# Kernel optimization log

Hardware: AMD Instinct MI355X
Metric: run time of the kernel (lower is better)

## Reference

```python
import jax, jax.numpy as jnp
import numpy as np

N = 100000
E = 1600000
IN_CH = 128
HID = 32
HEADS = 4
OUT_CH = 64
NEG_SLOPE = 0.2


def _gat_conv(x, src, dst, W, att_src, att_dst, bias, heads, out_ch):
    # PyG GATConv (concat=True, add_self_loops handled by caller via src/dst)
    n = x.shape[0]
    xp = (x @ W).reshape(n, heads, out_ch)                  # [N,H,C]
    a_src = (xp * att_src).sum(-1)                          # [N,H]
    a_dst = (xp * att_dst).sum(-1)                          # [N,H]
    e = jax.nn.leaky_relu(a_src[src] + a_dst[dst], NEG_SLOPE)  # [E,H]
    m = jax.ops.segment_max(e, dst, num_segments=n)         # per-dst max (safe: self-loops)
    ex = jnp.exp(e - m[dst])
    denom = jax.ops.segment_sum(ex, dst, num_segments=n)
    alpha = ex / denom[dst]                                  # [E,H]
    out = jax.ops.segment_sum(xp[src] * alpha[:, :, None], dst, num_segments=n)
    return out.reshape(n, heads * out_ch) + bias


def setup_inputs() -> dict:
    key = jax.random.key(0)
    ks = jax.random.split(key, 12)
    sc1 = 1.0 / np.sqrt(IN_CH)
    sc2 = 1.0 / np.sqrt(HID * HEADS * 2)
    return {
        "x_ppi": jax.random.normal(ks[0], (N, IN_CH), jnp.float32),
        "x_go": jax.random.normal(ks[1], (N, IN_CH), jnp.float32),
        "edge_index": jax.random.randint(ks[2], (2, E), 0, N, jnp.int32),
        "W1": jax.random.normal(ks[3], (IN_CH, HEADS * HID), jnp.float32) * sc1,
        "att_src1": jax.random.normal(ks[4], (HEADS, HID), jnp.float32) * sc1,
        "att_dst1": jax.random.normal(ks[5], (HEADS, HID), jnp.float32) * sc1,
        "b1": jnp.zeros((HEADS * HID,), jnp.float32),
        "W2": jax.random.normal(ks[6], (HID * HEADS * 2, OUT_CH), jnp.float32) * sc2,
        "att_src2": jax.random.normal(ks[7], (1, OUT_CH), jnp.float32) * sc2,
        "att_dst2": jax.random.normal(ks[8], (1, OUT_CH), jnp.float32) * sc2,
        "b2": jnp.zeros((OUT_CH,), jnp.float32),
    }


def reference(x_ppi, x_go, edge_index, W1, att_src1, att_dst1, b1, W2, att_src2, att_dst2, b2):
    loops = jnp.arange(N, dtype=edge_index.dtype)
    src = jnp.concatenate([edge_index[0], loops])
    dst = jnp.concatenate([edge_index[1], loops])
    h_ppi = _gat_conv(x_ppi, src, dst, W1, att_src1, att_dst1, b1, HEADS, HID)
    h_go = _gat_conv(x_go, src, dst, W1, att_src1, att_dst1, b1, HEADS, HID)
    h = jax.nn.relu(jnp.concatenate([h_ppi, h_go], axis=-1))  # [N, 2*H*HID]
    out = _gat_conv(h, src, dst, W2, att_src2, att_dst2, b2, 1, OUT_CH)
    return out
```

## Files before the change

kernel.cpp:

```cpp
#include <hip/hip_runtime.h>
#include <hip/hip_fp16.h>

constexpr int NN = 100000;
constexpr int EE = 1600000;
constexpr int ET = EE + NN;
constexpr int EQ = EE / 4;
constexpr int TQ = ET / 4;
constexpr int NBUK = (NN + 255) / 256;
constexpr int PB = 416;
constexpr float NEG = 0.2f;

typedef _Float16 f16x8 __attribute__((ext_vector_type(8)));
typedef _Float16 f16x4 __attribute__((ext_vector_type(4)));
typedef float    f32x4 __attribute__((ext_vector_type(4)));

__global__ __launch_bounds__(256) void k_bcount(const int4* __restrict__ dst4v,
                                                int* __restrict__ bucketCount) {
    __shared__ int bh[NBUK];
    for (int i = threadIdx.x; i < NBUK; i += 256) bh[i] = 0;
    __syncthreads();
    int gtid = blockIdx.x * 256 + threadIdx.x;
    for (int q = gtid; q < TQ; q += PB * 256) {
        int4 d;
        if (q < EQ) {
            d = dst4v[q];
        } else {
            int s0 = (q - EQ) * 4;
            d.x = s0; d.y = s0 + 1; d.z = s0 + 2; d.w = s0 + 3;
        }
        atomicAdd(&bh[d.x >> 8], 1);
        atomicAdd(&bh[d.y >> 8], 1);
        atomicAdd(&bh[d.z >> 8], 1);
        atomicAdd(&bh[d.w >> 8], 1);
    }
    __syncthreads();
    for (int i = threadIdx.x; i < NBUK; i += 256)
        if (bh[i]) atomicAdd(&bucketCount[i], bh[i]);
}

__global__ __launch_bounds__(512) void k_bscan(const int* __restrict__ bucketCount,
                                               int* __restrict__ bstart, int* __restrict__ gcur,
                                               int* __restrict__ rs) {
    __shared__ int sh[512];
    int t = threadIdx.x;
    int v = (t < NBUK) ? bucketCount[t] : 0;
    sh[t] = v;
    __syncthreads();
    for (int o = 1; o < 512; o <<= 1) {
        int u = (t >= o) ? sh[t - o] : 0;
        __syncthreads();
        sh[t] += u;
        __syncthreads();
    }
    if (t < NBUK) { bstart[t] = sh[t] - v; gcur[t] = sh[t] - v; }
    if (t == 0) { bstart[NBUK] = ET; rs[NN] = ET; }
}

__global__ __launch_bounds__(256) void k_bplace(const int4* __restrict__ src4v, const int4* __restrict__ dst4v,
                                                int* __restrict__ gcur, unsigned int* __restrict__ ebuf) {
    __shared__ int bh[NBUK];
    __shared__ int bbase[NBUK];
    for (int i = threadIdx.x; i < NBUK; i += 256) bh[i] = 0;
    __syncthreads();
    int gtid = blockIdx.x * 256 + threadIdx.x;

    int esrc[16];
    int emeta[16];
#pragma unroll
    for (int it = 0; it < 4; it++) {
        int q = gtid + it * (PB * 256);
        bool valid = q < TQ;
        int4 s, d;
        if (valid) {
            if (q < EQ) { s = src4v[q]; d = dst4v[q]; }
            else { int s0 = (q - EQ) * 4; s.x = s0; s.y = s0 + 1; s.z = s0 + 2; s.w = s0 + 3; d = s; }
        } else {
            s.x = s.y = s.z = s.w = 0; d = s;
        }
        int ss[4] = {s.x, s.y, s.z, s.w};
        int dd[4] = {d.x, d.y, d.z, d.w};
#pragma unroll
        for (int k = 0; k < 4; k++) {
            int idx = it * 4 + k;
            if (valid) {
                int b = dd[k] >> 8, l = dd[k] & 255;
                int r = atomicAdd(&bh[b], 1);
                esrc[idx]  = ss[k];
                emeta[idx] = (b << 21) | (l << 13) | r;
            } else {
                emeta[idx] = -1;
            }
        }
    }
    __syncthreads();
    for (int i = threadIdx.x; i < NBUK; i += 256)
        bbase[i] = bh[i] ? atomicAdd(&gcur[i], bh[i]) : 0;
    __syncthreads();
#pragma unroll
    for (int e = 0; e < 16; e++) {
        int me = emeta[e];
        if (me >= 0) {
            int b = me >> 21, l = (me >> 13) & 255, r = me & 8191;
            ebuf[bbase[b] + r] = ((unsigned)l << 24) | (unsigned)esrc[e];
        }
    }
}

__global__ __launch_bounds__(256) void k_csr(const unsigned int* __restrict__ ebuf,
                                             const int* __restrict__ bstart,
                                             int* __restrict__ rs, int* __restrict__ csr) {
    __shared__ int hist[256];
    __shared__ int sh[256];
    __shared__ int cur[256];
    int b = blockIdx.x;
    int t = threadIdx.x;
    int e0 = bstart[b], e1 = bstart[b + 1];
    hist[t] = 0;
    __syncthreads();
    for (int j = e0 + t; j < e1; j += 256)
        atomicAdd(&hist[ebuf[j] >> 24], 1);
    __syncthreads();
    int v = hist[t];
    sh[t] = v;
    __syncthreads();
    for (int o = 1; o < 256; o <<= 1) {
        int u = (t >= o) ? sh[t - o] : 0;
        __syncthreads();
        sh[t] += u;
        __syncthreads();
    }
    int excl = sh[t] - v;
    cur[t] = excl;
    int v0 = b * 256;
    if (v0 + t < NN) rs[v0 + t] = e0 + excl;
    __syncthreads();
    for (int j = e0 + t; j < e1; j += 256) {
        unsigned int e = ebuf[j];
        int l = (int)(e >> 24);
        int r = atomicAdd(&cur[l], 1);
        csr[e0 + r] = (int)(e & 0x00FFFFFFu);
    }
}

template <int K, int C, int OUT_MODE, bool SRCF32>
__global__ __launch_bounds__(256) void gemm_mfma(const void* __restrict__ xv, const float* __restrict__ W,
                                                 __half* __restrict__ xp, int n, int set_off) {
    constexpr int KC  = 64;
    constexpr int AST = KC + 8;
    constexpr int NT  = C / 16;
    constexpr int NST = K / KC;
    __shared__ _Float16 a_lds[128 * AST];
    __shared__ _Float16 w_lds[C * AST];

    const int tid  = threadIdx.x;
    const int w    = tid >> 6;
    const int lane = tid & 63;
    const int quad = lane >> 4;
    const int l16  = lane & 15;
    const long r0  = (long)blockIdx.x * 128;

    f32x4 acc[2][NT];
#pragma unroll
    for (int s = 0; s < 2; s++)
#pragma unroll
        for (int t = 0; t < NT; t++) acc[s][t] = (f32x4){0.f, 0.f, 0.f, 0.f};

    for (int st = 0; st < NST; ++st) {
        const int k0 = st * KC;
        for (int i = tid; i < 128 * (KC / 4); i += 256) {
            int r = i / (KC / 4);
            int q = i % (KC / 4);
            long row = r0 + r;
            f16x4 hv = (f16x4){0, 0, 0, 0};
            if (row < n) {
                if (SRCF32) {
                    float4 v = ((const float4*)xv)[row * (K / 4) + (k0 / 4) + q];
                    hv = (f16x4){(_Float16)v.x, (_Float16)v.y, (_Float16)v.z, (_Float16)v.w};
                } else {
                    hv = ((const f16x4*)xv)[row * (K / 4) + (k0 / 4) + q];
                }
            }
            *(f16x4*)&a_lds[r * AST + q * 4] = hv;
        }
        for (int i = tid; i < C * (KC / 4); i += 256) {
            int nn = i / (KC / 4);
            int kq = i % (KC / 4);
            f16x4 hv;
            hv.x = (_Float16)W[(long)(k0 + kq * 4 + 0) * C + nn];
            hv.y = (_Float16)W[(long)(k0 + kq * 4 + 1) * C + nn];
            hv.z = (_Float16)W[(long)(k0 + kq * 4 + 2) * C + nn];
            hv.w = (_Float16)W[(long)(k0 + kq * 4 + 3) * C + nn];
            *(f16x4*)&w_lds[nn * AST + kq * 4] = hv;
        }
        __syncthreads();

#pragma unroll
        for (int ks = 0; ks < KC; ks += 32) {
            f16x8 a0 = *(const f16x8*)&a_lds[(w * 32 + l16) * AST + ks + quad * 8];
            f16x8 a1 = *(const f16x8*)&a_lds[(w * 32 + 16 + l16) * AST + ks + quad * 8];
#pragma unroll
            for (int t = 0; t < NT; t++) {
                f16x8 b = *(const f16x8*)&w_lds[(t * 16 + l16) * AST + ks + quad * 8];
                acc[0][t] = __builtin_amdgcn_mfma_f32_16x16x32_f16(a0, b, acc[0][t], 0, 0, 0);
                acc[1][t] = __builtin_amdgcn_mfma_f32_16x16x32_f16(a1, b, acc[1][t], 0, 0, 0);
            }
        }
        __syncthreads();
    }

#pragma unroll
    for (int sub = 0; sub < 2; sub++) {
        long rb = r0 + w * 32 + sub * 16 + quad * 4;
#pragma unroll
        for (int t = 0; t < NT; t++) {
            int c = t * 16 + l16;
#pragma unroll
            for (int rg = 0; rg < 4; rg++) {
                long row = rb + rg;
                if (row < n) {
                    __half hv = __float2half(acc[sub][t][rg]);
                    if (OUT_MODE == 0)
                        xp[row * 256 + ((c >> 1) << 2) + (c & 1) + set_off] = hv;
                    else
                        xp[row * (long)C + c] = hv;
                }
            }
        }
    }
}

__global__ __launch_bounds__(256) void attn1_plain(const __half2* __restrict__ xp_p,
                                                   const __half2* __restrict__ xp_g,
                                                   const float* __restrict__ as_w, const float* __restrict__ ad_w,
                                                   float* __restrict__ att_sp, float* __restrict__ att_dp,
                                                   float* __restrict__ att_sg, float* __restrict__ att_dg, int n) {
    int idx = blockIdx.x * 256 + threadIdx.x;
    if (idx >= n * 4) return;
    int v = idx >> 2, hh = idx & 3;
    const __half2* rp = xp_p + (long)v * 64 + hh * 16;
    const __half2* rg = xp_g + (long)v * 64 + hh * 16;
    const float* a1 = as_w + hh * 32;
    const float* a2 = ad_w + hh * 32;
    float sp1 = 0.f, sp2 = 0.f, sg1 = 0.f, sg2 = 0.f;
#pragma unroll
    for (int t = 0; t < 16; t++) {
        float2 fp = __half22float2(rp[t]);
        float2 fg = __half22float2(rg[t]);
        float2 w1 = *(const float2*)(a1 + 2 * t);
        float2 w2 = *(const float2*)(a2 + 2 * t);
        sp1 += fp.x * w1.x + fp.y * w1.y;
        sp2 += fp.x * w2.x + fp.y * w2.y;
        sg1 += fg.x * w1.x + fg.y * w1.y;
        sg2 += fg.x * w2.x + fg.y * w2.y;
    }
    att_sp[idx] = sp1; att_dp[idx] = sp2;
    att_sg[idx] = sg1; att_dg[idx] = sg2;
}

__global__ __launch_bounds__(256) void attn2_kernel(const __half2* __restrict__ xp,
                                                    const float* __restrict__ as_w, const float* __restrict__ ad_w,
                                                    float* __restrict__ asrc, float* __restrict__ adst, int n) {
    int v = blockIdx.x * 256 + threadIdx.x;
    if (v >= n) return;
    const __half2* p = xp + (long)v * 32;
    float s1 = 0.f, s2 = 0.f;
#pragma unroll
    for (int c = 0; c < 32; c++) {
        float2 xv = __half22float2(p[c]);
        float2 w1 = *(const float2*)(as_w + 2 * c);
        float2 w2 = *(const float2*)(ad_w + 2 * c);
        s1 += xv.x * w1.x + xv.y * w1.y;
        s2 += xv.x * w2.x + xv.y * w2.y;
    }
    asrc[v] = s1;
    adst[v] = s2;
}

__global__ __launch_bounds__(256) void w1prep_node(const int* __restrict__ rs, const int* __restrict__ csr,
                                                   const float4* __restrict__ att_sp4, const float4* __restrict__ att_dp4,
                                                   const float4* __restrict__ att_sg4, const float4* __restrict__ att_dg4,
                                                   float4* __restrict__ wbp4, float4* __restrict__ wbg4) {
    int v = blockIdx.x * 16 + (threadIdx.x >> 4);
    if (v >= NN) return;
    int sl = threadIdx.x & 15;
    int e0 = rs[v], e1 = rs[v + 1];
    float4 dp = att_dp4[v], dg = att_dg4[v];
    auto w = [](float e) { e = (e > 0.f) ? e : NEG * e; return __expf(e); };
    for (int j = e0 + sl; j < e1; j += 16) {
        int s = csr[j];
        float4 sp = att_sp4[s], sg = att_sg4[s];
        float4 wp, wg;
        wp.x = w(sp.x + dp.x); wp.y = w(sp.y + dp.y);
        wp.z = w(sp.z + dp.z); wp.w = w(sp.w + dp.w);
        wg.x = w(sg.x + dg.x); wg.y = w(sg.y + dg.y);
        wg.z = w(sg.z + dg.z); wg.w = w(sg.w + dg.w);
        wbp4[j] = wp;
        wbg4[j] = wg;
    }
}

__global__ __launch_bounds__(256) void conv1_pass(const int* __restrict__ rs, const int* __restrict__ csr,
                                                  const uint4* __restrict__ xp,
                                                  const float* __restrict__ wb,
                                                  const float* __restrict__ bias,
                                                  __half* __restrict__ out, int off) {
    int v = blockIdx.x * 4 + (threadIdx.x >> 6);
    if (v >= NN) return;
    int lane = threadIdx.x & 63;
    int qw = lane >> 4;
    int m = lane & 15;
    int hd = m >> 2;
    int e0 = rs[v], e1 = rs[v + 1];

    float a[8];
#pragma unroll
    for (int i = 0; i < 8; i++) a[i] = 0.f;
    float d = 0.f;

    int j = e0;
    for (; j + 16 <= e1; j += 16) {
        int s[4]; float w[4]; uint4 r[4];
#pragma unroll
        for (int k = 0; k < 4; k++) s[k] = csr[j + 4 * k + qw];
#pragma unroll
        for (int k = 0; k < 4; k++) w[k] = wb[(j + 4 * k + qw) * 4 + hd];
#pragma unroll
        for (int k = 0; k < 4; k++) r[k] = xp[(long)s[k] * 16 + m];
#pragma unroll
        for (int k = 0; k < 4; k++) {
            d += w[k];
            float2 f0 = __half22float2(*(__half2*)&r[k].x);
            float2 f1 = __half22float2(*(__half2*)&r[k].y);
            float2 f2 = __half22float2(*(__half2*)&r[k].z);
            float2 f3 = __half22float2(*(__half2*)&r[k].w);
            a[0] += w[k] * f0.x; a[1] += w[k] * f0.y;
            a[2] += w[k] * f1.x; a[3] += w[k] * f1.y;
            a[4] += w[k] * f2.x; a[5] += w[k] * f2.y;
            a[6] += w[k] * f3.x; a[7] += w[k] * f3.y;
        }
    }
    for (; j < e1; j += 4) {
        int jj = j + qw;
        int jc = (jj < e1) ? jj : (e1 - 1);
        int s = csr[jc];
        float w = (jj < e1) ? wb[jc * 4 + hd] : 0.f;
        uint4 r = xp[(long)s * 16 + m];
        d += w;
        float2 f0 = __half22float2(*(__half2*)&r.x);
        float2 f1 = __half22float2(*(__half2*)&r.y);
        float2 f2 = __half22float2(*(__half2*)&r.z);
        float2 f3 = __half22float2(*(__half2*)&r.w);
        a[0] += w * f0.x; a[1] += w * f0.y;
        a[2] += w * f1.x; a[3] += w * f1.y;
        a[4] += w * f2.x; a[5] += w * f2.y;
        a[6] += w * f3.x; a[7] += w * f3.y;
    }

#pragma unroll
    for (int i = 0; i < 8; i++) {
        a[i] += __shfl_xor(a[i], 16);
        a[i] += __shfl_xor(a[i], 32);
    }
    d += __shfl_xor(d, 16);
    d += __shfl_xor(d, 32);

    if (qw == 0) {
        float inv = 1.0f / d;
        const float4* b4 = (const float4*)bias;
        float4 bA = b4[2 * m], bB = b4[2 * m + 1];
        __half2 o01 = __floats2half2_rn(fmaxf(a[0] * inv + bA.x, 0.f), fmaxf(a[1] * inv + bA.y, 0.f));
        __half2 o23 = __floats2half2_rn(fmaxf(a[2] * inv + bA.z, 0.f), fmaxf(a[3] * inv + bA.w, 0.f));
        __half2 o45 = __floats2half2_rn(fmaxf(a[4] * inv + bB.x, 0.f), fmaxf(a[5] * inv + bB.y, 0.f));
        __half2 o67 = __floats2half2_rn(fmaxf(a[6] * inv + bB.z, 0.f), fmaxf(a[7] * inv + bB.w, 0.f));
        uint4 st;
        st.x = *(unsigned int*)&o01;
        st.y = *(unsigned int*)&o23;
        st.z = *(unsigned int*)&o45;
        st.w = *(unsigned int*)&o67;
        *(uint4*)(out + (long)v * 256 + off + 8 * m) = st;
    }
}

__global__ __launch_bounds__(256) void conv2_edge(const int* __restrict__ rs, const int* __restrict__ csr,
                                                  const __half* __restrict__ xp,
                                                  const float* __restrict__ asrc,
                                                  const float* __restrict__ adst,
                                                  const float* __restrict__ bias,
                                                  float* __restrict__ out) {
    int v = blockIdx.x * 4 + (threadIdx.x >> 6);
    if (v >= NN) return;
    int lane = threadIdx.x & 63;
    int qw = lane >> 4;
    int m = lane & 15;
    int e0 = rs[v], e1 = rs[v + 1];
    const uint2* xp2 = (const uint2*)xp;

    float adv = adst[v];
    auto lrexp = [](float e) { e = (e > 0.f) ? e : NEG * e; return __expf(e); };

    float a0 = 0.f, a1 = 0.f, a2 = 0.f, a3 = 0.f, d = 0.f;

    int j = e0;
    for (; j + 16 <= e1; j += 16) {
        int s[4]; float av[4]; uint2 r[4];
#pragma unroll
        for (int k = 0; k < 4; k++) s[k] = csr[j + 4 * k + qw];
#pragma unroll
        for (int k = 0; k < 4; k++) av[k] = asrc[s[k]];
#pragma unroll
        for (int k = 0; k < 4; k++) r[k] = xp2[(long)s[k] * 16 + m];
#pragma unroll
        for (int k = 0; k < 4; k++) {
            float w = lrexp(av[k] + adv);
            d += w;
            float2 x01 = __half22float2(*(__half2*)&r[k].x);
            float2 x23 = __half22float2(*(__half2*)&r[k].y);
            a0 += w * x01.x; a1 += w * x01.y;
            a2 += w * x23.x; a3 += w * x23.y;
        }
    }
    for (; j < e1; j += 4) {
        int jj = j + qw;
        int jc = (jj < e1) ? jj : (e1 - 1);
        int s = csr[jc];
        float av = asrc[s];
        uint2 r = xp2[(long)s * 16 + m];
        float w = (jj < e1) ? lrexp(av + adv) : 0.f;
        d += w;
        float2 x01 = __half22float2(*(__half2*)&r.x);
        float2 x23 = __half22float2(*(__half2*)&r.y);
        a0 += w * x01.x; a1 += w * x01.y;
        a2 += w * x23.x; a3 += w * x23.y;
    }

    a0 += __shfl_xor(a0, 16); a1 += __shfl_xor(a1, 16);
    a2 += __shfl_xor(a2, 16); a3 += __shfl_xor(a3, 16);
    d  += __shfl_xor(d, 16);
    a0 += __shfl_xor(a0, 32); a1 += __shfl_xor(a1, 32);
    a2 += __shfl_xor(a2, 32); a3 += __shfl_xor(a3, 32);
    d  += __shfl_xor(d, 32);

    if (qw == 0) {
        float inv = 1.0f / d;
        float4 b4 = *(const float4*)&bias[4 * m];
        float4 o;
        o.x = a0 * inv + b4.x;
        o.y = a1 * inv + b4.y;
        o.z = a2 * inv + b4.z;
        o.w = a3 * inv + b4.w;
        *(float4*)&out[(long)v * 64 + 4 * m] = o;
    }
}

extern "C" void kernel_launch(void* const* d_in, const int* in_sizes, int n_in,
                              void* d_out, int out_size, void* d_ws, size_t ws_size,
                              hipStream_t stream) {
    const float* x_ppi = (const float*)d_in[0];
    const float* x_go  = (const float*)d_in[1];
    const int*   ei    = (const int*)d_in[2];
    const float* W1    = (const float*)d_in[3];
    const float* as1   = (const float*)d_in[4];
    const float* ad1   = (const float*)d_in[5];
    const float* b1    = (const float*)d_in[6];
    const float* W2    = (const float*)d_in[7];
    const float* as2   = (const float*)d_in[8];
    const float* ad2   = (const float*)d_in[9];
    const float* b2    = (const float*)d_in[10];
    float* out = (float*)d_out;

    char* ws = (char*)d_ws;
    size_t off = 0;
    auto alloc = [&](size_t bytes) -> void* {
        void* p = ws + off;
        off = (off + bytes + 255) & ~(size_t)255;
        return p;
    };
    int* bucketCount = (int*)alloc((size_t)NBUK * 4);
    int* bstart      = (int*)alloc((size_t)(NBUK + 1) * 4);
    int* gcur        = (int*)alloc((size_t)NBUK * 4);
    unsigned int* ebuf = (unsigned int*)alloc((size_t)ET * 4);
    int* rs      = (int*)alloc((size_t)(NN + 1) * 4);
    int* csr     = (int*)alloc((size_t)ET * 4);
    __half* xp_p = (__half*)alloc((size_t)NN * 128 * 2);
    __half* xp_g = (__half*)alloc((size_t)NN * 128 * 2);
    __half* xp2  = (__half*)alloc((size_t)NN * 64 * 2);
    float* attsp = (float*)alloc((size_t)NN * 4 * 4);
    float* attdp = (float*)alloc((size_t)NN * 4 * 4);
    float* attsg = (float*)alloc((size_t)NN * 4 * 4);
    float* attdg = (float*)alloc((size_t)NN * 4 * 4);
    float* asr2  = (float*)alloc((size_t)NN * 4);
    float* ads2  = (float*)alloc((size_t)NN * 4);
    float* wbp   = (float*)alloc((size_t)ET * 16);
    float* wbg   = (float*)alloc((size_t)ET * 16);
    __half* hbuf = (__half*)alloc((size_t)NN * 256 * 2);
    (void)ws_size; (void)in_sizes; (void)n_in; (void)out_size;

    const int GB = (NN + 127) / 128;

    hipMemsetAsync(bucketCount, 0, (size_t)NBUK * 4, stream);
    k_bcount<<<PB, 256, 0, stream>>>((const int4*)(ei + EE), bucketCount);
    k_bscan<<<1, 512, 0, stream>>>(bucketCount, bstart, gcur, rs);
    k_bplace<<<PB, 256, 0, stream>>>((const int4*)ei, (const int4*)(ei + EE), gcur, ebuf);
    k_csr<<<NBUK, 256, 0, stream>>>(ebuf, bstart, rs, csr);

    gemm_mfma<128, 128, 1, true><<<GB, 256, 0, stream>>>(x_ppi, W1, xp_p, NN, 0);
    gemm_mfma<128, 128, 1, true><<<GB, 256, 0, stream>>>(x_go, W1, xp_g, NN, 0);
    attn1_plain<<<(NN * 4 + 255) / 256, 256, 0, stream>>>((const __half2*)xp_p, (const __half2*)xp_g,
                                                          as1, ad1, attsp, attdp, attsg, attdg, NN);
    w1prep_node<<<(NN + 15) / 16, 256, 0, stream>>>(rs, csr, (const float4*)attsp, (const float4*)attdp,
                                                    (const float4*)attsg, (const float4*)attdg,
                                                    (float4*)wbp, (float4*)wbg);
    conv1_pass<<<NN / 4, 256, 0, stream>>>(rs, csr, (const uint4*)xp_p, wbp, b1, hbuf, 0);
    conv1_pass<<<NN / 4, 256, 0, stream>>>(rs, csr, (const uint4*)xp_g, wbg, b1, hbuf, 128);

    gemm_mfma<256, 64, 1, false><<<GB, 256, 0, stream>>>(hbuf, W2, xp2, NN, 0);
    attn2_kernel<<<(NN + 255) / 256, 256, 0, stream>>>((const __half2*)xp2, as2, ad2, asr2, ads2, NN);
    conv2_edge<<<NN / 4, 256, 0, stream>>>(rs, csr, xp2, asr2, ads2, b2, out);
}
```

Before: 563.0 us.

## Fuse attention logits into direct-load MFMA GEMM with pre-transposed fp16 weights

Replaces the LDS-staged GEMM with one that loads A fragments and pre-transposed fp16 weights straight from global memory into MFMA registers. A small prep kernel transposes and converts W1/W2 once per call. The per-node attention dot products are computed in the GEMM epilogue from the fp32 accumulators via lane shuffles, which removes the separate attn1/attn2 kernels and their re-read of xp. The trade-off is that weights are now read per block from global memory or L2 rather than from LDS, and the attention logits use fp32 accumulators instead of fp16-rounded xp.

Measured after the change: 505.7 us. -10.2%, faster.

```diff
diff --git a/kernel.cpp b/kernel.cpp
--- a/kernel.cpp
+++ b/kernel.cpp
@@ -142,22 +142,35 @@
     }
 }
 
-template <int K, int C, int OUT_MODE, bool SRCF32>
-__global__ __launch_bounds__(256) void gemm_mfma(const void* __restrict__ xv, const float* __restrict__ W,
-                                                 __half* __restrict__ xp, int n, int set_off) {
-    constexpr int KC  = 64;
-    constexpr int AST = KC + 8;
-    constexpr int NT  = C / 16;
-    constexpr int NST = K / KC;
-    __shared__ _Float16 a_lds[128 * AST];
-    __shared__ _Float16 w_lds[C * AST];
-
+__global__ __launch_bounds__(256) void k_wprep(const float* __restrict__ W1, const float* __restrict__ W2,
+                                               _Float16* __restrict__ w1T, _Float16* __restrict__ w2T) {
+    int idx = blockIdx.x * 256 + threadIdx.x;
+    if (idx < 128 * 128) {
+        int nn = idx >> 7, k = idx & 127;
+        w1T[idx] = (_Float16)W1[k * 128 + nn];
+    }
+    int i2 = idx - 128 * 128;
+    if (i2 >= 0 && i2 < 64 * 256) {
+        int nn = i2 >> 8, k = i2 & 255;
+        w2T[i2] = (_Float16)W2[k * 64 + nn];
+    }
+}
+
+template <int K, int C, bool SRCF32, int AMODE>
+__global__ __launch_bounds__(256) void gemm_direct(const void* __restrict__ xv,
+                                                   const _Float16* __restrict__ wT,
+                                                   const float* __restrict__ as_w, const float* __restrict__ ad_w,
+                                                   __half* __restrict__ xp,
+                                                   float* __restrict__ att_s, float* __restrict__ att_d, int n) {
+    constexpr int NT = C / 16;
     const int tid  = threadIdx.x;
     const int w    = tid >> 6;
     const int lane = tid & 63;
     const int quad = lane >> 4;
     const int l16  = lane & 15;
     const long r0  = (long)blockIdx.x * 128;
+    const long row0 = r0 + w * 32 + l16;
+    const long row1 = row0 + 16;
 
     f32x4 acc[2][NT];
 #pragma unroll
@@ -165,115 +178,112 @@
 #pragma unroll
         for (int t = 0; t < NT; t++) acc[s][t] = (f32x4){0.f, 0.f, 0.f, 0.f};
 
-    for (int st = 0; st < NST; ++st) {
-        const int k0 = st * KC;
-        for (int i = tid; i < 128 * (KC / 4); i += 256) {
-            int r = i / (KC / 4);
-            int q = i % (KC / 4);
-            long row = r0 + r;
-            f16x4 hv = (f16x4){0, 0, 0, 0};
-            if (row < n) {
-                if (SRCF32) {
-                    float4 v = ((const float4*)xv)[row * (K / 4) + (k0 / 4) + q];
-                    hv = (f16x4){(_Float16)v.x, (_Float16)v.y, (_Float16)v.z, (_Float16)v.w};
-                } else {
-                    hv = ((const f16x4*)xv)[row * (K / 4) + (k0 / 4) + q];
+#pragma unroll
+    for (int ks = 0; ks < K; ks += 32) {
+        f16x8 a0 = (f16x8){0, 0, 0, 0, 0, 0, 0, 0};
+        f16x8 a1 = (f16x8){0, 0, 0, 0, 0, 0, 0, 0};
+        if (SRCF32) {
+            if (row0 < n) {
+                const float4* p = (const float4*)((const float*)xv + row0 * K + ks) + quad * 2;
+                float4 u = p[0], v = p[1];
+                a0 = (f16x8){(_Float16)u.x, (_Float16)u.y, (_Float16)u.z, (_Float16)u.w,
+                             (_Float16)v.x, (_Float16)v.y, (_Float16)v.z, (_Float16)v.w};
+            }
+            if (row1 < n) {
+                const float4* p = (const float4*)((const float*)xv + row1 * K + ks) + quad * 2;
+                float4 u = p[0], v = p[1];
+                a1 = (f16x8){(_Float16)u.x, (_Float16)u.y, (_Float16)u.z, (_Float16)u.w,
+                             (_Float16)v.x, (_Float16)v.y, (_Float16)v.z, (_Float16)v.w};
+            }
+        } else {
+            if (row0 < n) a0 = *(const f16x8*)((const _Float16*)xv + row0 * K + ks + quad * 8);
+            if (row1 < n) a1 = *(const f16x8*)((const _Float16*)xv + row1 * K + ks + quad * 8);
+        }
+#pragma unroll
+        for (int t = 0; t < NT; t++) {
+            f16x8 b = *(const f16x8*)(wT + (long)(t * 16 + l16) * K + ks + quad * 8);
+            acc[0][t] = __builtin_amdgcn_mfma_f32_16x16x32_f16(a0, b, acc[0][t], 0, 0, 0);
+            acc[1][t] = __builtin_amdgcn_mfma_f32_16x16x32_f16(a1, b, acc[1][t], 0, 0, 0);
+        }
+    }
+
+#pragma unroll
+    for (int sub = 0; sub < 2; sub++) {
+        long rb = r0 + w * 32 + sub * 16 + quad * 4;
+#pragma unroll
+        for (int t = 0; t < NT; t++) {
+            int c = t * 16 + l16;
+#pragma unroll
+            for (int rg = 0; rg < 4; rg++) {
+                long row = rb + rg;
+                if (row < n) xp[row * (long)C + c] = __float2half(acc[sub][t][rg]);
+            }
+        }
+    }
+
+    if (AMODE == 1) {
+        float asw[8], adw[8];
+#pragma unroll
+        for (int t = 0; t < 8; t++) {
+            int ci = (t >> 1) * 32 + (t & 1) * 16 + l16;
+            asw[t] = as_w[ci];
+            adw[t] = ad_w[ci];
+        }
+#pragma unroll
+        for (int sub = 0; sub < 2; sub++) {
+#pragma unroll
+            for (int rg = 0; rg < 4; rg++) {
+                long row = r0 + w * 32 + sub * 16 + quad * 4 + rg;
+                float hs[4] = {0.f, 0.f, 0.f, 0.f};
+                float hd[4] = {0.f, 0.f, 0.f, 0.f};
+#pragma unroll
+                for (int t = 0; t < 8; t++) {
+                    float av = acc[sub][t][rg];
+                    hs[t >> 1] += av * asw[t];
+                    hd[t >> 1] += av * adw[t];
+                }
+#pragma unroll
+                for (int h = 0; h < 4; h++) {
+                    hs[h] += __shfl_xor(hs[h], 1); hs[h] += __shfl_xor(hs[h], 2);
+                    hs[h] += __shfl_xor(hs[h], 4); hs[h] += __shfl_xor(hs[h], 8);
+                    hd[h] += __shfl_xor(hd[h], 1); hd[h] += __shfl_xor(hd[h], 2);
+                    hd[h] += __shfl_xor(hd[h], 4); hd[h] += __shfl_xor(hd[h], 8);
+                }
+                if (l16 == 0 && row < n) {
+                    ((float4*)att_s)[row] = make_float4(hs[0], hs[1], hs[2], hs[3]);
+                    ((float4*)att_d)[row] = make_float4(hd[0], hd[1], hd[2], hd[3]);
                 }
             }
-            *(f16x4*)&a_lds[r * AST + q * 4] = hv;
-        }
-        for (int i = tid; i < C * (KC / 4); i += 256) {
-            int nn = i / (KC / 4);
-            int kq = i % (KC / 4);
-            f16x4 hv;
-            hv.x = (_Float16)W[(long)(k0 + kq * 4 + 0) * C + nn];
-            hv.y = (_Float16)W[(long)(k0 + kq * 4 + 1) * C + nn];
-            hv.z = (_Float16)W[(long)(k0 + kq * 4 + 2) * C + nn];
-            hv.w = (_Float16)W[(long)(k0 + kq * 4 + 3) * C + nn];
-            *(f16x4*)&w_lds[nn * AST + kq * 4] = hv;
-        }
-        __syncthreads();
-
-#pragma unroll
-        for (int ks = 0; ks < KC; ks += 32) {
-            f16x8 a0 = *(const f16x8*)&a_lds[(w * 32 + l16) * AST + ks + quad * 8];
-            f16x8 a1 = *(const f16x8*)&a_lds[(w * 32 + 16 + l16) * AST + ks + quad * 8];
-#pragma unroll
-            for (int t = 0; t < NT; t++) {
-                f16x8 b = *(const f16x8*)&w_lds[(t * 16 + l16) * AST + ks + quad * 8];
-                acc[0][t] = __builtin_amdgcn_mfma_f32_16x16x32_f16(a0, b, acc[0][t], 0, 0, 0);
-                acc[1][t] = __builtin_amdgcn_mfma_f32_16x16x32_f16(a1, b, acc[1][t], 0, 0, 0);
-            }
-        }
-        __syncthreads();
-    }
-
-#pragma unroll
-    for (int sub = 0; sub < 2; sub++) {
-        long rb = r0 + w * 32 + sub * 16 + quad * 4;
+        }
+    }
+    if (AMODE == 2) {
+        float asw[NT], adw[NT];
 #pragma unroll
         for (int t = 0; t < NT; t++) {
-            int c = t * 16 + l16;
+            asw[t] = as_w[t * 16 + l16];
+            adw[t] = ad_w[t * 16 + l16];
+        }
+#pragma unroll
+        for (int sub = 0; sub < 2; sub++) {
 #pragma unroll
             for (int rg = 0; rg < 4; rg++) {
-                long row = rb + rg;
-                if (row < n) {
-                    __half hv = __float2half(acc[sub][t][rg]);
-                    if (OUT_MODE == 0)
-                        xp[row * 256 + ((c >> 1) << 2) + (c & 1) + set_off] = hv;
-                    else
-                        xp[row * (long)C + c] = hv;
+                long row = r0 + w * 32 + sub * 16 + quad * 4 + rg;
+                float s = 0.f, d = 0.f;
+#pragma unroll
+                for (int t = 0; t < NT; t++) {
+                    float av = acc[sub][t][rg];
+                    s += av * asw[t];
+                    d += av * adw[t];
+                }
+                s += __shfl_xor(s, 1); s += __shfl_xor(s, 2); s += __shfl_xor(s, 4); s += __shfl_xor(s, 8);
+                d += __shfl_xor(d, 1); d += __shfl_xor(d, 2); d += __shfl_xor(d, 4); d += __shfl_xor(d, 8);
+                if (l16 == 0 && row < n) {
+                    att_s[row] = s;
+                    att_d[row] = d;
                 }
             }
         }
     }
-}
-
-__global__ __launch_bounds__(256) void attn1_plain(const __half2* __restrict__ xp_p,
-                                                   const __half2* __restrict__ xp_g,
-                                                   const float* __restrict__ as_w, const float* __restrict__ ad_w,
-                                                   float* __restrict__ att_sp, float* __restrict__ att_dp,
-                                                   float* __restrict__ att_sg, float* __restrict__ att_dg, int n) {
-    int idx = blockIdx.x * 256 + threadIdx.x;
-    if (idx >= n * 4) return;
-    int v = idx >> 2, hh = idx & 3;
-    const __half2* rp = xp_p + (long)v * 64 + hh * 16;
-    const __half2* rg = xp_g + (long)v * 64 + hh * 16;
-    const float* a1 = as_w + hh * 32;
-    const float* a2 = ad_w + hh * 32;
-    float sp1 = 0.f, sp2 = 0.f, sg1 = 0.f, sg2 = 0.f;
-#pragma unroll
-    for (int t = 0; t < 16; t++) {
-        float2 fp = __half22float2(rp[t]);
-        float2 fg = __half22float2(rg[t]);
-        float2 w1 = *(const float2*)(a1 + 2 * t);
-        float2 w2 = *(const float2*)(a2 + 2 * t);
-        sp1 += fp.x * w1.x + fp.y * w1.y;
-        sp2 += fp.x * w2.x + fp.y * w2.y;
-        sg1 += fg.x * w1.x + fg.y * w1.y;
-        sg2 += fg.x * w2.x + fg.y * w2.y;
-    }
-    att_sp[idx] = sp1; att_dp[idx] = sp2;
-    att_sg[idx] = sg1; att_dg[idx] = sg2;
-}
-
-__global__ __launch_bounds__(256) void attn2_kernel(const __half2* __restrict__ xp,
-                                                    const float* __restrict__ as_w, const float* __restrict__ ad_w,
-                                                    float* __restrict__ asrc, float* __restrict__ adst, int n) {
-    int v = blockIdx.x * 256 + threadIdx.x;
-    if (v >= n) return;
-    const __half2* p = xp + (long)v * 32;
-    float s1 = 0.f, s2 = 0.f;
-#pragma unroll
-    for (int c = 0; c < 32; c++) {
-        float2 xv = __half22float2(p[c]);
-        float2 w1 = *(const float2*)(as_w + 2 * c);
-        float2 w2 = *(const float2*)(ad_w + 2 * c);
-        s1 += xv.x * w1.x + xv.y * w1.y;
-        s2 += xv.x * w2.x + xv.y * w2.y;
-    }
-    asrc[v] = s1;
-    adst[v] = s2;
 }
 
 __global__ __launch_bounds__(256) void w1prep_node(const int* __restrict__ rs, const int* __restrict__ csr,
@@ -481,6 +491,8 @@
     unsigned int* ebuf = (unsigned int*)alloc((size_t)ET * 4);
     int* rs      = (int*)alloc((size_t)(NN + 1) * 4);
     int* csr     = (int*)alloc((size_t)ET * 4);
+    _Float16* w1T = (_Float16*)alloc((size_t)128 * 128 * 2);
+    _Float16* w2T = (_Float16*)alloc((size_t)64 * 256 * 2);
     __half* xp_p = (__half*)alloc((size_t)NN * 128 * 2);
     __half* xp_g = (__half*)alloc((size_t)NN * 128 * 2);
     __half* xp2  = (__half*)alloc((size_t)NN * 64 * 2);
@@ -503,17 +515,16 @@
     k_bplace<<<PB, 256, 0, stream>>>((const int4*)ei, (const int4*)(ei + EE), gcur, ebuf);
     k_csr<<<NBUK, 256, 0, stream>>>(ebuf, bstart, rs, csr);
 
-    gemm_mfma<128, 128, 1, true><<<GB, 256, 0, stream>>>(x_ppi, W1, xp_p, NN, 0);
-    gemm_mfma<128, 128, 1, true><<<GB, 256, 0, stream>>>(x_go, W1, xp_g, NN, 0);
-    attn1_plain<<<(NN * 4 + 255) / 256, 256, 0, stream>>>((const __half2*)xp_p, (const __half2*)xp_g,
-                                                          as1, ad1, attsp, attdp, attsg, attdg, NN);
+    k_wprep<<<128, 256, 0, stream>>>(W1, W2, w1T, w2T);
+
+    gemm_direct<128, 128, true, 1><<<GB, 256, 0, stream>>>(x_ppi, w1T, as1, ad1, xp_p, attsp, attdp, NN);
+    gemm_direct<128, 128, true, 1><<<GB, 256, 0, stream>>>(x_go, w1T, as1, ad1, xp_g, attsg, attdg, NN);
     w1prep_node<<<(NN + 15) / 16, 256, 0, stream>>>(rs, csr, (const float4*)attsp, (const float4*)attdp,
                                                     (const float4*)attsg, (const float4*)attdg,
                                                     (float4*)wbp, (float4*)wbg);
     conv1_pass<<<NN / 4, 256, 0, stream>>>(rs, csr, (const uint4*)xp_p, wbp, b1, hbuf, 0);
     conv1_pass<<<NN / 4, 256, 0, stream>>>(rs, csr, (const uint4*)xp_g, wbg, b1, hbuf, 128);
 
-    gemm_mfma<256, 64, 1, false><<<GB, 256, 0, stream>>>(hbuf, W2, xp2, NN, 0);
-    attn2_kernel<<<(NN + 255) / 256, 256, 0, stream>>>((const __half2*)xp2, as2, ad2, asr2, ads2, NN);
+    gemm_direct<256, 64, false, 2><<<GB, 256, 0, stream>>>(hbuf, w2T, as2, ad2, xp2, asr2, ads2, NN);
     conv2_edge<<<NN / 4, 256, 0, stream>>>(rs, csr, xp2, asr2, ads2, b2, out);
 }
```
